# Kernel optimization log

Hardware: AMD Instinct MI355X
Metric: run time of the kernel (lower is better)

Reference implementation:

```python
import jax, jax.numpy as jnp
import numpy as np

N_VOX = 200000
Z, Y, X = 41, 256, 256


def _build_rulebook(N, seed=0):
    """Build submanifold 3x3x3 rulebook: nbr[i,k] = voxel index of neighbor k of voxel i, or -1."""
    rng = np.random.default_rng(seed)
    keys = np.unique(rng.integers(0, Z * Y * X, size=int(N * 1.3)))
    assert keys.shape[0] >= N
    keys = keys[:N]  # sorted unique linearized coords
    z = keys // (Y * X)
    rem = keys % (Y * X)
    y = rem // X
    x = rem % X
    nbr = np.full((N, 27), -1, np.int32)
    k = 0
    for dz in (-1, 0, 1):
        for dy in (-1, 0, 1):
            for dx in (-1, 0, 1):
                nz, ny, nx = z + dz, y + dy, x + dx
                valid = (nz >= 0) & (nz < Z) & (ny >= 0) & (ny < Y) & (nx >= 0) & (nx < X)
                nkey = (nz * Y + ny) * X + nx
                pos = np.searchsorted(keys, nkey)
                pos_c = np.minimum(pos, N - 1)
                found = valid & (keys[pos_c] == nkey)
                nbr[:, k] = np.where(found, pos_c, -1)
                k += 1
    return nbr


def setup_inputs() -> dict:
    key = jax.random.key(0)
    ks = jax.random.split(key, 8)
    nbr = jnp.asarray(_build_rulebook(N_VOX))
    return {
        "voxel_features": jax.random.normal(ks[0], (N_VOX, 4), jnp.float32),
        "nbr_idx": nbr,
        "W0": jax.random.normal(ks[1], (27, 4, 16), jnp.float32) * 0.05,
        "s0": jnp.ones((16,), jnp.float32),
        "b0": jnp.zeros((16,), jnp.float32),
        "W1": jax.random.normal(ks[2], (27, 16, 16), jnp.float32) * 0.05,
        "s1": jnp.ones((16,), jnp.float32),
        "b1": jnp.zeros((16,), jnp.float32),
        "W2": jax.random.normal(ks[3], (27, 16, 16), jnp.float32) * 0.05,
        "s2": jnp.ones((16,), jnp.float32),
        "b2": jnp.zeros((16,), jnp.float32),
        "W_lin": jax.random.normal(ks[4], (16, 3), jnp.float32) * 0.05,
        "b_lin": jnp.zeros((3,), jnp.float32),
    }


def _subm_conv(feats, W, nbr, mask):
    # feats: [N, Cin], W: [27, Cin, Cout], nbr: [N, 27] (rulebook), mask: [N, 27, 1]
    g = jnp.take(feats, jnp.maximum(nbr, 0), axis=0) * mask  # [N, 27, Cin] gather (memory-bound)
    return jnp.einsum("nkc,kcd->nd", g, W)  # scatter-free dense contraction


def reference(voxel_features, nbr_idx, W0, s0, b0, W1, s1, b1, W2, s2, b2, W_lin, b_lin):
    mask = (nbr_idx >= 0)[..., None].astype(voxel_features.dtype)
    # conv_input: SubMConv3d(4,16,3) + BN(folded to scale/shift) + ReLU
    x = jax.nn.relu(_subm_conv(voxel_features, W0, nbr_idx, mask) * s0 + b0)
    # SparseBasicBlock(16,16, indice_key='subm1'): conv-bn-relu-conv-bn + residual + relu
    idn = x
    h = jax.nn.relu(_subm_conv(x, W1, nbr_idx, mask) * s1 + b1)
    h = _subm_conv(h, W2, nbr_idx, mask) * s2 + b2
    x = jax.nn.relu(h + idn)
    # mos_seg_layer: Linear(16, mos_class)
    return x @ W_lin + b_lin
```

## Files before the change

kernel.cpp:

```cpp
#include <hip/hip_runtime.h>

#define NVOX 200000

__device__ __forceinline__ void fma16x16(const float4* __restrict__ wrow,
                                         float4 f0, float4 f1, float4 f2, float4 f3,
                                         float acc[16]) {
    const float g[16] = {f0.x, f0.y, f0.z, f0.w, f1.x, f1.y, f1.z, f1.w,
                         f2.x, f2.y, f2.z, f2.w, f3.x, f3.y, f3.z, f3.w};
    #pragma unroll
    for (int cc = 0; cc < 16; ++cc) {
        float gc = g[cc];
        float4 w0 = wrow[cc * 4 + 0];
        float4 w1 = wrow[cc * 4 + 1];
        float4 w2 = wrow[cc * 4 + 2];
        float4 w3 = wrow[cc * 4 + 3];
        acc[0]  += gc * w0.x; acc[1]  += gc * w0.y; acc[2]  += gc * w0.z; acc[3]  += gc * w0.w;
        acc[4]  += gc * w1.x; acc[5]  += gc * w1.y; acc[6]  += gc * w1.z; acc[7]  += gc * w1.w;
        acc[8]  += gc * w2.x; acc[9]  += gc * w2.y; acc[10] += gc * w2.z; acc[11] += gc * w2.w;
        acc[12] += gc * w3.x; acc[13] += gc * w3.y; acc[14] += gc * w3.z; acc[15] += gc * w3.w;
    }
}

__global__ __launch_bounds__(256) void k1_compact_conv0(
    const float* __restrict__ feats,
    const int* __restrict__ nbr,
    const float* __restrict__ W,
    const float* __restrict__ s, const float* __restrict__ b,
    int* __restrict__ ent,
    int* __restrict__ cnt,
    float* __restrict__ x) {
    __shared__ int   lnbr[256 * 27];
    __shared__ float Wl[27 * 68];
    int t = threadIdx.x;
    int base = blockIdx.x * 256;
    for (int i = t; i < 27 * 64; i += 256)
        Wl[(i >> 6) * 68 + (i & 63)] = W[i];
    int nv = NVOX - base; if (nv > 256) nv = 256;
    int count = nv * 27;
    const int* gsrc = nbr + base * 27;
    for (int i = t; i < count; i += 256)
        lnbr[i] = gsrc[i];
    __syncthreads();

    int n = base + t;
    if (n >= NVOX) return;
    int* row = lnbr + t * 27;
    int c = 0;
    #pragma unroll
    for (int k = 0; k < 27; ++k) {
        int idx = row[k];
        if (idx >= 0) {
            int e = (idx << 5) | k;
            row[c] = e;
            ent[c * NVOX + n] = e;
            ++c;
        }
    }
    cnt[n] = c;

    float acc[16];
    #pragma unroll
    for (int d = 0; d < 16; ++d) acc[d] = 0.f;
    int e = row[0];
    float4 f = *(const float4*)(feats + (e >> 5) * 4);
    int j = 0;
    while (true) {
        bool more = (++j < c);
        int en = e; float4 fn = f;
        if (more) {
            en = row[j];
            fn = *(const float4*)(feats + (en >> 5) * 4);
        }
        {
            const float4* wrow = (const float4*)(Wl + (e & 31) * 68);
            float g[4] = {f.x, f.y, f.z, f.w};
            #pragma unroll
            for (int cc = 0; cc < 4; ++cc) {
                float gc = g[cc];
                float4 w0 = wrow[cc * 4 + 0];
                float4 w1 = wrow[cc * 4 + 1];
                float4 w2 = wrow[cc * 4 + 2];
                float4 w3 = wrow[cc * 4 + 3];
                acc[0]  += gc * w0.x; acc[1]  += gc * w0.y; acc[2]  += gc * w0.z; acc[3]  += gc * w0.w;
                acc[4]  += gc * w1.x; acc[5]  += gc * w1.y; acc[6]  += gc * w1.z; acc[7]  += gc * w1.w;
                acc[8]  += gc * w2.x; acc[9]  += gc * w2.y; acc[10] += gc * w2.z; acc[11] += gc * w2.w;
                acc[12] += gc * w3.x; acc[13] += gc * w3.y; acc[14] += gc * w3.z; acc[15] += gc * w3.w;
            }
        }
        if (!more) break;
        e = en; f = fn;
    }
    float4* o = (float4*)(x + n * 16);
    #pragma unroll
    for (int q = 0; q < 4; ++q) {
        float4 r;
        float v0 = acc[q * 4 + 0] * s[q * 4 + 0] + b[q * 4 + 0];
        float v1 = acc[q * 4 + 1] * s[q * 4 + 1] + b[q * 4 + 1];
        float v2 = acc[q * 4 + 2] * s[q * 4 + 2] + b[q * 4 + 2];
        float v3 = acc[q * 4 + 3] * s[q * 4 + 3] + b[q * 4 + 3];
        r.x = v0 > 0.f ? v0 : 0.f;
        r.y = v1 > 0.f ? v1 : 0.f;
        r.z = v2 > 0.f ? v2 : 0.f;
        r.w = v3 > 0.f ? v3 : 0.f;
        o[q] = r;
    }
}

__device__ __forceinline__ void conv16_core(const float* __restrict__ fin,
                                            const int* __restrict__ ent,
                                            int c, int n, const float* Wl,
                                            float acc[16]) {
    int e = ent[n];
    const float4* fp = (const float4*)(fin + (e >> 5) * 16);
    float4 f0 = fp[0], f1 = fp[1], f2 = fp[2], f3 = fp[3];
    int j = 0;
    while (true) {
        bool more = (++j < c);
        int en = e;
        float4 g0 = f0, g1 = f1, g2 = f2, g3 = f3;
        if (more) {
            en = ent[j * NVOX + n];
            const float4* fq = (const float4*)(fin + (en >> 5) * 16);
            g0 = fq[0]; g1 = fq[1]; g2 = fq[2]; g3 = fq[3];
        }
        fma16x16((const float4*)(Wl + (e & 31) * 260), f0, f1, f2, f3, acc);
        if (!more) break;
        e = en; f0 = g0; f1 = g1; f2 = g2; f3 = g3;
    }
}

__global__ __launch_bounds__(256) void k2_conv1(
    const float* __restrict__ fin,
    const int* __restrict__ ent, const int* __restrict__ cnt,
    const float* __restrict__ W,
    const float* __restrict__ s, const float* __restrict__ b,
    float* __restrict__ out) {
    __shared__ float Wl[27 * 260];
    for (int i = threadIdx.x; i < 27 * 256; i += 256)
        Wl[(i >> 8) * 260 + (i & 255)] = W[i];
    __syncthreads();
    int n = blockIdx.x * 256 + threadIdx.x;
    if (n >= NVOX) return;
    int c = cnt[n];
    float acc[16];
    #pragma unroll
    for (int d = 0; d < 16; ++d) acc[d] = 0.f;
    conv16_core(fin, ent, c, n, Wl, acc);
    float4* o = (float4*)(out + n * 16);
    #pragma unroll
    for (int q = 0; q < 4; ++q) {
        float4 r;
        float v0 = acc[q * 4 + 0] * s[q * 4 + 0] + b[q * 4 + 0];
        float v1 = acc[q * 4 + 1] * s[q * 4 + 1] + b[q * 4 + 1];
        float v2 = acc[q * 4 + 2] * s[q * 4 + 2] + b[q * 4 + 2];
        float v3 = acc[q * 4 + 3] * s[q * 4 + 3] + b[q * 4 + 3];
        r.x = v0 > 0.f ? v0 : 0.f;
        r.y = v1 > 0.f ? v1 : 0.f;
        r.z = v2 > 0.f ? v2 : 0.f;
        r.w = v3 > 0.f ? v3 : 0.f;
        o[q] = r;
    }
}

__global__ __launch_bounds__(256) void k3_conv2_final(
    const float* __restrict__ fin,
    const int* __restrict__ ent, const int* __restrict__ cnt,
    const float* __restrict__ W,
    const float* __restrict__ s, const float* __restrict__ b,
    const float* __restrict__ idn,
    const float* __restrict__ Wlin,
    const float* __restrict__ blin,
    float* __restrict__ out) {
    __shared__ float Wl[27 * 260];
    for (int i = threadIdx.x; i < 27 * 256; i += 256)
        Wl[(i >> 8) * 260 + (i & 255)] = W[i];
    __syncthreads();
    int n = blockIdx.x * 256 + threadIdx.x;
    if (n >= NVOX) return;
    int c = cnt[n];
    float acc[16];
    #pragma unroll
    for (int d = 0; d < 16; ++d) acc[d] = 0.f;
    conv16_core(fin, ent, c, n, Wl, acc);
    const float4* ip = (const float4*)(idn + n * 16);
    float4 i0 = ip[0], i1 = ip[1], i2 = ip[2], i3 = ip[3];
    float id[16] = {i0.x, i0.y, i0.z, i0.w, i1.x, i1.y, i1.z, i1.w,
                    i2.x, i2.y, i2.z, i2.w, i3.x, i3.y, i3.z, i3.w};
    float o0 = blin[0], o1 = blin[1], o2 = blin[2];
    #pragma unroll
    for (int d = 0; d < 16; ++d) {
        float v = acc[d] * s[d] + b[d] + id[d];
        v = v > 0.f ? v : 0.f;
        o0 += v * Wlin[d * 3 + 0];
        o1 += v * Wlin[d * 3 + 1];
        o2 += v * Wlin[d * 3 + 2];
    }
    out[n * 3 + 0] = o0;
    out[n * 3 + 1] = o1;
    out[n * 3 + 2] = o2;
}

extern "C" void kernel_launch(void* const* d_in, const int* in_sizes, int n_in,
                              void* d_out, int out_size, void* d_ws, size_t ws_size,
                              hipStream_t stream) {
    const float* feats = (const float*)d_in[0];
    const int*   nbr   = (const int*)d_in[1];
    const float* W0    = (const float*)d_in[2];
    const float* s0    = (const float*)d_in[3];
    const float* b0    = (const float*)d_in[4];
    const float* W1    = (const float*)d_in[5];
    const float* s1    = (const float*)d_in[6];
    const float* b1    = (const float*)d_in[7];
    const float* W2    = (const float*)d_in[8];
    const float* s2    = (const float*)d_in[9];
    const float* b2    = (const float*)d_in[10];
    const float* Wlin  = (const float*)d_in[11];
    const float* blin  = (const float*)d_in[12];
    float* out = (float*)d_out;

    char* ws = (char*)d_ws;
    int*   ent = (int*)(ws);
    int*   cnt = (int*)(ws + 21600000);
    float* x   = (float*)(ws + 22400000);
    float* h   = (float*)(ws + 35200000);

    int blocks = (NVOX + 255) / 256;
    k1_compact_conv0<<<blocks, 256, 0, stream>>>(feats, nbr, W0, s0, b0, ent, cnt, x);
    k2_conv1<<<blocks, 256, 0, stream>>>(x, ent, cnt, W1, s1, b1, h);
    k3_conv2_final<<<blocks, 256, 0, stream>>>(h, ent, cnt, W2, s2, b2, x, Wlin, blin, out);
}
```

Baseline: 67.66 us.

## Store intermediates in fp16, use dot2 with 4 threads per voxel and sorted counts

Intermediate activations x and h are now stored as packed fp16, which halves gather traffic. The 16x16 contractions use v_dot2 fp16 instructions against weights pre-packed by a new pack kernel. Conv1 and conv2 now assign 4 threads per voxel, each covering 4 output channels, and voxels inside a block are ranked by neighbor count to reduce divergence. Block sizes change as well. The cost is reduced precision in the intermediates, plus an extra kernel launch and a ranking pass.

```diff
diff --git a/kernel.cpp b/kernel.cpp
--- a/kernel.cpp
+++ b/kernel.cpp
@@ -1,49 +1,59 @@
 #include <hip/hip_runtime.h>
+#include <cstdint>
 
 #define NVOX 200000
-
-__device__ __forceinline__ void fma16x16(const float4* __restrict__ wrow,
-                                         float4 f0, float4 f1, float4 f2, float4 f3,
-                                         float acc[16]) {
-    const float g[16] = {f0.x, f0.y, f0.z, f0.w, f1.x, f1.y, f1.z, f1.w,
-                         f2.x, f2.y, f2.z, f2.w, f3.x, f3.y, f3.z, f3.w};
-    #pragma unroll
-    for (int cc = 0; cc < 16; ++cc) {
-        float gc = g[cc];
-        float4 w0 = wrow[cc * 4 + 0];
-        float4 w1 = wrow[cc * 4 + 1];
-        float4 w2 = wrow[cc * 4 + 2];
-        float4 w3 = wrow[cc * 4 + 3];
-        acc[0]  += gc * w0.x; acc[1]  += gc * w0.y; acc[2]  += gc * w0.z; acc[3]  += gc * w0.w;
-        acc[4]  += gc * w1.x; acc[5]  += gc * w1.y; acc[6]  += gc * w1.z; acc[7]  += gc * w1.w;
-        acc[8]  += gc * w2.x; acc[9]  += gc * w2.y; acc[10] += gc * w2.z; acc[11] += gc * w2.w;
-        acc[12] += gc * w3.x; acc[13] += gc * w3.y; acc[14] += gc * w3.z; acc[15] += gc * w3.w;
-    }
-}
-
-__global__ __launch_bounds__(256) void k1_compact_conv0(
+#define T1 128
+#define NT1 ((NVOX + T1 - 1) / T1)
+#define VPB 64
+#define NT2 ((NVOX + VPB - 1) / VPB)
+#define WPITCH 132
+
+typedef _Float16 h2 __attribute__((ext_vector_type(2)));
+
+__device__ __forceinline__ uint32_t packh2(float a, float b) {
+    h2 v; v.x = (_Float16)a; v.y = (_Float16)b;
+    return __builtin_bit_cast(uint32_t, v);
+}
+__device__ __forceinline__ h2 toh2(uint32_t u) { return __builtin_bit_cast(h2, u); }
+
+__global__ __launch_bounds__(256) void k0_pack(const float* __restrict__ W1,
+                                               const float* __restrict__ W2,
+                                               uint32_t* __restrict__ wp1,
+                                               uint32_t* __restrict__ wp2) {
+    int i = blockIdx.x * 256 + threadIdx.x;
+    if (i >= 2 * 3456) return;
+    int half = i >= 3456;
+    int r = i - half * 3456;
+    const float* W = half ? W2 : W1;
+    uint32_t* wp = half ? wp2 : wp1;
+    int k = r >> 7, j = r & 127, d = j >> 3, p = j & 7;
+    float a = W[(k * 16 + 2 * p) * 16 + d];
+    float b = W[(k * 16 + 2 * p + 1) * 16 + d];
+    wp[r] = packh2(a, b);
+}
+
+__global__ __launch_bounds__(128) void k1_compact_conv0(
     const float* __restrict__ feats,
     const int* __restrict__ nbr,
     const float* __restrict__ W,
     const float* __restrict__ s, const float* __restrict__ b,
     int* __restrict__ ent,
     int* __restrict__ cnt,
-    float* __restrict__ x) {
-    __shared__ int   lnbr[256 * 27];
-    __shared__ float Wl[27 * 68];
+    uint32_t* __restrict__ xh) {
+    __shared__ int   lnbr[T1 * 27];
+    __shared__ __align__(16) float Wl[27 * 68];
     int t = threadIdx.x;
-    int base = blockIdx.x * 256;
-    for (int i = t; i < 27 * 64; i += 256)
+    int base = blockIdx.x * T1;
+    for (int i = t; i < 27 * 64; i += T1)
         Wl[(i >> 6) * 68 + (i & 63)] = W[i];
-    int nv = NVOX - base; if (nv > 256) nv = 256;
-    int count = nv * 27;
+    int nv = NVOX - base; if (nv > T1) nv = T1;
     const int* gsrc = nbr + base * 27;
-    for (int i = t; i < count; i += 256)
+    for (int i = t; i < nv * 27; i += T1)
         lnbr[i] = gsrc[i];
     __syncthreads();
 
     int n = base + t;
-    if (n >= NVOX) return;
+    if (t >= nv) return;
     int* row = lnbr + t * 27;
     int c = 0;
     #pragma unroll
@@ -90,114 +100,172 @@
         if (!more) break;
         e = en; f = fn;
     }
-    float4* o = (float4*)(x + n * 16);
-    #pragma unroll
-    for (int q = 0; q < 4; ++q) {
-        float4 r;
-        float v0 = acc[q * 4 + 0] * s[q * 4 + 0] + b[q * 4 + 0];
-        float v1 = acc[q * 4 + 1] * s[q * 4 + 1] + b[q * 4 + 1];
-        float v2 = acc[q * 4 + 2] * s[q * 4 + 2] + b[q * 4 + 2];
-        float v3 = acc[q * 4 + 3] * s[q * 4 + 3] + b[q * 4 + 3];
-        r.x = v0 > 0.f ? v0 : 0.f;
-        r.y = v1 > 0.f ? v1 : 0.f;
-        r.z = v2 > 0.f ? v2 : 0.f;
-        r.w = v3 > 0.f ? v3 : 0.f;
-        o[q] = r;
-    }
-}
-
-__device__ __forceinline__ void conv16_core(const float* __restrict__ fin,
+    float v[16];
+    #pragma unroll
+    for (int d = 0; d < 16; ++d) {
+        float u = acc[d] * s[d] + b[d];
+        v[d] = u > 0.f ? u : 0.f;
+    }
+    uint4 u0, u1;
+    u0.x = packh2(v[0], v[1]);  u0.y = packh2(v[2], v[3]);
+    u0.z = packh2(v[4], v[5]);  u0.w = packh2(v[6], v[7]);
+    u1.x = packh2(v[8], v[9]);  u1.y = packh2(v[10], v[11]);
+    u1.z = packh2(v[12], v[13]); u1.w = packh2(v[14], v[15]);
+    ((uint4*)xh)[n * 2 + 0] = u0;
+    ((uint4*)xh)[n * 2 + 1] = u1;
+}
+
+__device__ __forceinline__ void conv16_dot2(const uint32_t* __restrict__ fin,
                                             const int* __restrict__ ent,
-                                            int c, int n, const float* Wl,
-                                            float acc[16]) {
+                                            int c, int n, int d0,
+                                            const uint32_t* __restrict__ wl,
+                                            float acc[4]) {
+    #pragma unroll
+    for (int d = 0; d < 4; ++d) acc[d] = 0.f;
+    if (c <= 0) return;
     int e = ent[n];
-    const float4* fp = (const float4*)(fin + (e >> 5) * 16);
-    float4 f0 = fp[0], f1 = fp[1], f2 = fp[2], f3 = fp[3];
+    const uint4* fp = (const uint4*)(fin + (e >> 5) * 8);
+    uint4 fa = fp[0], fb = fp[1];
     int j = 0;
     while (true) {
         bool more = (++j < c);
         int en = e;
-        float4 g0 = f0, g1 = f1, g2 = f2, g3 = f3;
+        uint4 ga = fa, gb = fb;
         if (more) {
             en = ent[j * NVOX + n];
-            const float4* fq = (const float4*)(fin + (en >> 5) * 16);
-            g0 = fq[0]; g1 = fq[1]; g2 = fq[2]; g3 = fq[3];
-        }
-        fma16x16((const float4*)(Wl + (e & 31) * 260), f0, f1, f2, f3, acc);
+            const uint4* fq = (const uint4*)(fin + (en >> 5) * 8);
+            ga = fq[0]; gb = fq[1];
+        }
+        {
+            int k = e & 31;
+            h2 f0 = toh2(fa.x), f1 = toh2(fa.y), f2 = toh2(fa.z), f3 = toh2(fa.w);
+            h2 f4 = toh2(fb.x), f5 = toh2(fb.y), f6 = toh2(fb.z), f7 = toh2(fb.w);
+            const uint32_t* wk = wl + k * WPITCH + d0 * 8;
+            #pragma unroll
+            for (int dd = 0; dd < 4; ++dd) {
+                uint4 wa = *(const uint4*)(wk + dd * 8);
+                uint4 wb = *(const uint4*)(wk + dd * 8 + 4);
+                float a = acc[dd];
+                a = __builtin_amdgcn_fdot2(f0, toh2(wa.x), a, false);
+                a = __builtin_amdgcn_fdot2(f1, toh2(wa.y), a, false);
+                a = __builtin_amdgcn_fdot2(f2, toh2(wa.z), a, false);
+                a = __builtin_amdgcn_fdot2(f3, toh2(wa.w), a, false);
+                a = __builtin_amdgcn_fdot2(f4, toh2(wb.x), a, false);
+                a = __builtin_amdgcn_fdot2(f5, toh2(wb.y), a, false);
+                a = __builtin_amdgcn_fdot2(f6, toh2(wb.z), a, false);
+                a = __builtin_amdgcn_fdot2(f7, toh2(wb.w), a, false);
+                acc[dd] = a;
+            }
+        }
         if (!more) break;
-        e = en; f0 = g0; f1 = g1; f2 = g2; f3 = g3;
-    }
-}
-
-__global__ __launch_bounds__(256) void k2_conv1(
-    const float* __restrict__ fin,
+        e = en; fa = ga; fb = gb;
+    }
+}
+
+__device__ __forceinline__ void stage_and_rank(const uint32_t* __restrict__ wp,
+                                               const int* __restrict__ cnt,
+                                               uint32_t* __restrict__ wl,
+                                               int* __restrict__ lcnt, int* __restrict__ lperm,
+                                               int base, int t) {
+    for (int i = t; i < 3456; i += 256)
+        wl[(i >> 7) * WPITCH + (i & 127)] = wp[i];
+    if (t < VPB) {
+        int n = base + t;
+        lcnt[t] = (n < NVOX) ? cnt[n] : 0;
+    }
+    __syncthreads();
+    if (t < VPB) {
+        int me = lcnt[t];
+        int r = 0;
+        #pragma unroll 8
+        for (int j2 = 0; j2 < VPB; ++j2) {
+            int oj = lcnt[j2];
+            r += (oj < me) || (oj == me && j2 < t);
+        }
+        lperm[r] = t;
+    }
+    __syncthreads();
+}
+
+__global__ __launch_bounds__(256, 6) void k2_conv1(
+    const uint32_t* __restrict__ xh,
     const int* __restrict__ ent, const int* __restrict__ cnt,
-    const float* __restrict__ W,
+    const uint32_t* __restrict__ wp,
     const float* __restrict__ s, const float* __restrict__ b,
-    float* __restrict__ out) {
-    __shared__ float Wl[27 * 260];
-    for (int i = threadIdx.x; i < 27 * 256; i += 256)
-        Wl[(i >> 8) * 260 + (i & 255)] = W[i];
-    __syncthreads();
-    int n = blockIdx.x * 256 + threadIdx.x;
-    if (n >= NVOX) return;
-    int c = cnt[n];
-    float acc[16];
-    #pragma unroll
-    for (int d = 0; d < 16; ++d) acc[d] = 0.f;
-    conv16_core(fin, ent, c, n, Wl, acc);
-    float4* o = (float4*)(out + n * 16);
-    #pragma unroll
-    for (int q = 0; q < 4; ++q) {
-        float4 r;
-        float v0 = acc[q * 4 + 0] * s[q * 4 + 0] + b[q * 4 + 0];
-        float v1 = acc[q * 4 + 1] * s[q * 4 + 1] + b[q * 4 + 1];
-        float v2 = acc[q * 4 + 2] * s[q * 4 + 2] + b[q * 4 + 2];
-        float v3 = acc[q * 4 + 3] * s[q * 4 + 3] + b[q * 4 + 3];
-        r.x = v0 > 0.f ? v0 : 0.f;
-        r.y = v1 > 0.f ? v1 : 0.f;
-        r.z = v2 > 0.f ? v2 : 0.f;
-        r.w = v3 > 0.f ? v3 : 0.f;
-        o[q] = r;
-    }
-}
-
-__global__ __launch_bounds__(256) void k3_conv2_final(
-    const float* __restrict__ fin,
+    uint32_t* __restrict__ hh) {
+    __shared__ __align__(16) uint32_t wl[27 * WPITCH];
+    __shared__ int lcnt[VPB];
+    __shared__ int lperm[VPB];
+    int t = threadIdx.x;
+    int base = blockIdx.x * VPB;
+    stage_and_rank(wp, cnt, wl, lcnt, lperm, base, t);
+    int g = t >> 2, cg = t & 3;
+    int lv = lperm[g];
+    int n = base + lv;
+    bool valid = n < NVOX;
+    int c = lcnt[lv];
+    int d0 = cg * 4;
+    float acc[4];
+    conv16_dot2(xh, ent, valid ? c : 0, n, d0, wl, acc);
+    if (!valid) return;
+    float v[4];
+    #pragma unroll
+    for (int dd = 0; dd < 4; ++dd) {
+        float u = acc[dd] * s[d0 + dd] + b[d0 + dd];
+        v[dd] = u > 0.f ? u : 0.f;
+    }
+    uint2 o;
+    o.x = packh2(v[0], v[1]);
+    o.y = packh2(v[2], v[3]);
+    *(uint2*)(hh + n * 8 + cg * 2) = o;
+}
+
+__global__ __launch_bounds__(256, 6) void k3_conv2_final(
+    const uint32_t* __restrict__ hh,
     const int* __restrict__ ent, const int* __restrict__ cnt,
-    const float* __restrict__ W,
+    const uint32_t* __restrict__ wp,
     const float* __restrict__ s, const float* __restrict__ b,
-    const float* __restrict__ idn,
+    const uint32_t* __restrict__ xh,
     const float* __restrict__ Wlin,
     const float* __restrict__ blin,
     float* __restrict__ out) {
-    __shared__ float Wl[27 * 260];
-    for (int i = threadIdx.x; i < 27 * 256; i += 256)
-        Wl[(i >> 8) * 260 + (i & 255)] = W[i];
-    __syncthreads();
-    int n = blockIdx.x * 256 + threadIdx.x;
-    if (n >= NVOX) return;
-    int c = cnt[n];
-    float acc[16];
-    #pragma unroll
-    for (int d = 0; d < 16; ++d) acc[d] = 0.f;
-    conv16_core(fin, ent, c, n, Wl, acc);
-    const float4* ip = (const float4*)(idn + n * 16);
-    float4 i0 = ip[0], i1 = ip[1], i2 = ip[2], i3 = ip[3];
-    float id[16] = {i0.x, i0.y, i0.z, i0.w, i1.x, i1.y, i1.z, i1.w,
-                    i2.x, i2.y, i2.z, i2.w, i3.x, i3.y, i3.z, i3.w};
-    float o0 = blin[0], o1 = blin[1], o2 = blin[2];
-    #pragma unroll
-    for (int d = 0; d < 16; ++d) {
-        float v = acc[d] * s[d] + b[d] + id[d];
-        v = v > 0.f ? v : 0.f;
-        o0 += v * Wlin[d * 3 + 0];
-        o1 += v * Wlin[d * 3 + 1];
-        o2 += v * Wlin[d * 3 + 2];
-    }
-    out[n * 3 + 0] = o0;
-    out[n * 3 + 1] = o1;
-    out[n * 3 + 2] = o2;
+    __shared__ __align__(16) uint32_t wl[27 * WPITCH];
+    __shared__ int lcnt[VPB];
+    __shared__ int lperm[VPB];
+    int t = threadIdx.x;
+    int base = blockIdx.x * VPB;
+    stage_and_rank(wp, cnt, wl, lcnt, lperm, base, t);
+    int g = t >> 2, cg = t & 3;
+    int lv = lperm[g];
+    int n = base + lv;
+    bool valid = n < NVOX;
+    int c = lcnt[lv];
+    int d0 = cg * 4;
+    float acc[4];
+    conv16_dot2(hh, ent, valid ? c : 0, n, d0, wl, acc);
+    float o0 = 0.f, o1 = 0.f, o2 = 0.f;
+    if (valid) {
+        uint2 iv = *(const uint2*)(xh + n * 8 + cg * 2);
+        h2 i0 = toh2(iv.x), i1 = toh2(iv.y);
+        float idn[4] = {(float)i0.x, (float)i0.y, (float)i1.x, (float)i1.y};
+        #pragma unroll
+        for (int dd = 0; dd < 4; ++dd) {
+            int d = d0 + dd;
+            float u = acc[dd] * s[d] + b[d] + idn[dd];
+            u = u > 0.f ? u : 0.f;
+            o0 += u * Wlin[d * 3 + 0];
+            o1 += u * Wlin[d * 3 + 1];
+            o2 += u * Wlin[d * 3 + 2];
+        }
+    }
+    o0 += __shfl_xor(o0, 1); o0 += __shfl_xor(o0, 2);
+    o1 += __shfl_xor(o1, 1); o1 += __shfl_xor(o1, 2);
+    o2 += __shfl_xor(o2, 1); o2 += __shfl_xor(o2, 2);
+    if (valid && cg == 0) {
+        out[n * 3 + 0] = o0 + blin[0];
+        out[n * 3 + 1] = o1 + blin[1];
+        out[n * 3 + 2] = o2 + blin[2];
+    }
 }
 
 extern "C" void kernel_launch(void* const* d_in, const int* in_sizes, int n_in,
@@ -219,13 +287,15 @@
     float* out = (float*)d_out;
 
     char* ws = (char*)d_ws;
-    int*   ent = (int*)(ws);
-    int*   cnt = (int*)(ws + 21600000);
-    float* x   = (float*)(ws + 22400000);
-    float* h   = (float*)(ws + 35200000);
-
-    int blocks = (NVOX + 255) / 256;
-    k1_compact_conv0<<<blocks, 256, 0, stream>>>(feats, nbr, W0, s0, b0, ent, cnt, x);
-    k2_conv1<<<blocks, 256, 0, stream>>>(x, ent, cnt, W1, s1, b1, h);
-    k3_conv2_final<<<blocks, 256, 0, stream>>>(h, ent, cnt, W2, s2, b2, x, Wlin, blin, out);
-}
+    int*      ent = (int*)(ws);
+    int*      cnt = (int*)(ws + 21600000);
+    uint32_t* xh  = (uint32_t*)(ws + 22400000);
+    uint32_t* hh  = (uint32_t*)(ws + 28800000);
+    uint32_t* wp1 = (uint32_t*)(ws + 35200000);
+    uint32_t* wp2 = (uint32_t*)(ws + 35213824);
+
+    k0_pack<<<27, 256, 0, stream>>>(W1, W2, wp1, wp2);
+    k1_compact_conv0<<<NT1, T1, 0, stream>>>(feats, nbr, W0, s0, b0, ent, cnt, xh);
+    k2_conv1<<<NT2, 256, 0, stream>>>(xh, ent, cnt, wp1, s1, b1, hh);
+    k3_conv2_final<<<NT2, 256, 0, stream>>>(hh, ent, cnt, wp2, s2, b2, xh, Wlin, blin, out);
+}
```

New measurement: 76.94 us. 13.7% more time.
